# Kernel tuning notes

Hardware: AMD Instinct MI355X
Metric: run time of the kernel (lower is better)

The kernel has to match this reference:

```python
import jax, jax.numpy as jnp
import numpy as np

H, E, N, R = 1024, 2048, 16, 64  # hidden, expand, state, dt_rank
B, L = 2, 2048


def setup_inputs() -> dict:
    key = jax.random.key(0)
    ks = jax.random.split(key, 20)
    s = 0.02
    inp = {
        "x": jax.random.normal(ks[0], (B, L, H), jnp.float32),
        "ln_gamma": jnp.ones((H,), jnp.float32),
        "ln_beta": jnp.zeros((H,), jnp.float32),
        "W_in": jax.random.normal(ks[1], (H, 2 * E), jnp.float32) * s,
        "b_in": jnp.zeros((2 * E,), jnp.float32),
        "W_delta": jax.random.normal(ks[2], (E, R), jnp.float32) * s,
        "b_delta": jnp.zeros((R,), jnp.float32),
        "W_dt": jax.random.normal(ks[3], (R, E), jnp.float32) * s,
        "b_dt": jnp.zeros((E,), jnp.float32),
        "W_B": jax.random.normal(ks[4], (E, N), jnp.float32) * s,
        "b_B": jnp.zeros((N,), jnp.float32),
        "W_C": jax.random.normal(ks[5], (E, N), jnp.float32) * s,
        "b_C": jnp.zeros((N,), jnp.float32),
        "A_log": -jnp.exp(jax.random.normal(ks[6], (E, N), jnp.float32) * 0.1),
        "D": jax.random.normal(ks[7], (E,), jnp.float32) * 0.1,
        "W_out": jax.random.normal(ks[8], (E, H), jnp.float32) * s,
        "b_out": jnp.zeros((H,), jnp.float32),
    }
    return inp


def _layer_norm(x, gamma, beta, eps=1e-5):
    mu = jnp.mean(x, axis=-1, keepdims=True)
    var = jnp.var(x, axis=-1, keepdims=True)
    return (x - mu) * jax.lax.rsqrt(var + eps) * gamma + beta


def _selective_scan(x, delta, A, Bm, Cm):
    # x, delta: [B,L,E]; Bm, Cm: [B,L,N]; A: [E,N]
    def step(h, inputs):
        x_t, d_t, B_t, C_t = inputs  # [B,E],[B,E],[B,N],[B,N]
        A_disc = jnp.exp(d_t[..., None] * A)                     # [B,E,N]
        h = A_disc * h + d_t[..., None] * B_t[:, None, :] * x_t[..., None]
        y_t = jnp.einsum('bn,ben->be', C_t, h)
        return h, y_t

    h0 = jnp.zeros((x.shape[0], A.shape[0], A.shape[1]), x.dtype)
    xs = (jnp.swapaxes(x, 0, 1), jnp.swapaxes(delta, 0, 1),
          jnp.swapaxes(Bm, 0, 1), jnp.swapaxes(Cm, 0, 1))
    _, ys = jax.lax.scan(step, h0, xs)  # ys: [L,B,E]
    return jnp.swapaxes(ys, 0, 1)


def reference(x, ln_gamma, ln_beta, W_in, b_in, W_delta, b_delta, W_dt, b_dt,
              W_B, b_B, W_C, b_C, A_log, D, W_out, b_out):
    residual = x
    xn = _layer_norm(x, ln_gamma, ln_beta)
    x_proj = xn @ W_in + b_in                     # [B,L,2E]
    u, gate = jnp.split(x_proj, 2, axis=-1)
    u = jax.nn.silu(u)
    delta = jax.nn.softplus((u @ W_delta + b_delta) @ W_dt + b_dt)  # [B,L,E]
    Bm = u @ W_B + b_B                            # [B,L,N]
    Cm = u @ W_C + b_C                            # [B,L,N]
    A = -jnp.exp(A_log)                           # [E,N]
    y = _selective_scan(u, delta, A, Bm, Cm)
    y = y + u * D
    y = y * jax.nn.silu(gate)
    return y @ W_out + b_out + residual
```

## Files before the change

kernel.cpp:

```cpp
#include <hip/hip_runtime.h>
#include <stdint.h>

#define DH 1024
#define DE 2048
#define DN 16
#define DR 64
#define DB 2
#define DL 2048
#define DT (DB * DL)

typedef short short8 __attribute__((ext_vector_type(8)));
typedef float f32x4 __attribute__((ext_vector_type(4)));

__device__ __forceinline__ float bf2f(uint32_t u) {
  union { uint32_t i; float f; } v; v.i = u << 16; return v.f;
}
__device__ __forceinline__ unsigned short f2bf(float f) {
  union { float f; uint32_t i; } v; v.f = f;
  uint32_t r = v.i + 0x7FFFu + ((v.i >> 16) & 1u);
  return (unsigned short)(r >> 16);
}
__device__ __forceinline__ float ldsc(const void* p, size_t i, bool f32) {
  return f32 ? ((const float*)p)[i] : bf2f(((const unsigned short*)p)[i]);
}
__device__ __forceinline__ float4 ld4(const void* p, size_t i, bool f32) {
  if (f32) return *(const float4*)((const float*)p + i);
  ushort4 v = *(const ushort4*)((const unsigned short*)p + i);
  return make_float4(bf2f(v.x), bf2f(v.y), bf2f(v.z), bf2f(v.w));
}

__device__ __forceinline__ void gll16(const unsigned short* g, unsigned short* l) {
  __builtin_amdgcn_global_load_lds(
      (const __attribute__((address_space(1))) unsigned int*)g,
      (__attribute__((address_space(3))) unsigned int*)l, 16, 0, 0);
}

__device__ __forceinline__ void transpose_tile(
    const void* src, unsigned short* dst, int K, int N, int bx, int by,
    int tid, bool f32, float (*tile)[33]) {
  const int tx = tid & 31;
  const int ty = tid >> 5;
  const int kb = by * 32, nb = bx * 32;
  #pragma unroll
  for (int i = 0; i < 4; ++i)
    tile[ty + 8 * i][tx] = ldsc(src, (size_t)(kb + ty + 8 * i) * N + nb + tx, f32);
  __syncthreads();
  #pragma unroll
  for (int i = 0; i < 4; ++i)
    dst[(size_t)(nb + ty + 8 * i) * K + kb + tx] = f2bf(tile[tx][ty + 8 * i]);
}

__global__ __launch_bounds__(256) void k_convert_all(
    const void* __restrict__ W_in, const void* __restrict__ W_out,
    const void* __restrict__ W_dt, const void* __restrict__ Wd,
    const void* __restrict__ Wb, const void* __restrict__ Wc,
    const void* __restrict__ b_in, const void* __restrict__ b_out,
    const void* __restrict__ b_delta, const void* __restrict__ b_B,
    const void* __restrict__ b_C, const void* __restrict__ A_log,
    const void* __restrict__ Dvec, const void* __restrict__ b_dt,
    unsigned short* __restrict__ WtIn, unsigned short* __restrict__ WtOut,
    unsigned short* __restrict__ WtDt, unsigned short* __restrict__ WtDbc,
    float* __restrict__ bin, float* __restrict__ bout,
    float* __restrict__ bdbc, float* __restrict__ Ac, float* __restrict__ Dv,
    float* __restrict__ bdt,
    const uint32_t* __restrict__ probe) {
  const bool f32 = (probe[0] == 0x3F800000u);
  __shared__ float tile[32][33];
  const int tid = threadIdx.x;
  int f = blockIdx.x;
  if (f < 4096) {
    transpose_tile(W_in, WtIn, 1024, 4096, f & 127, f >> 7, tid, f32, tile);
    return;
  }
  f -= 4096;
  if (f < 2048) {
    transpose_tile(W_out, WtOut, 2048, 1024, f & 31, f >> 5, tid, f32, tile);
    return;
  }
  f -= 2048;
  if (f < 128) {
    transpose_tile(W_dt, WtDt, 64, 2048, f & 63, f >> 6, tid, f32, tile);
    return;
  }
  f -= 128;
  if (f < 1024) {
    const int idx = f * 256 + tid;
    const int c = idx >> 11, k = idx & 2047;
    float v = 0.f;
    if (c < 64) v = ldsc(Wd, (size_t)k * DR + c, f32);
    else if (c < 80) v = ldsc(Wb, (size_t)k * DN + (c - 64), f32);
    else if (c < 96) v = ldsc(Wc, (size_t)k * DN + (c - 80), f32);
    WtDbc[idx] = f2bf(v);
    return;
  }
  f -= 1024;
  {
    int i = f * 256 + tid;
    if (i < 4096) { bin[i] = ldsc(b_in, i, f32); return; }
    i -= 4096;
    if (i < 1024) { bout[i] = ldsc(b_out, i, f32); return; }
    i -= 1024;
    if (i < 128) {
      float v = 0.f;
      if (i < 64) v = ldsc(b_delta, i, f32);
      else if (i < 80) v = ldsc(b_B, i - 64, f32);
      else if (i < 96) v = ldsc(b_C, i - 80, f32);
      bdbc[i] = v; return;
    }
    i -= 128;
    if (i < 32768) { Ac[i] = -__expf(ldsc(A_log, i, f32)); return; }
    i -= 32768;
    if (i < 2048) { Dv[i] = ldsc(Dvec, i, f32); return; }
    i -= 2048;
    if (i < 2048) { bdt[i] = ldsc(b_dt, i, f32); }
  }
}

__global__ __launch_bounds__(256) void k_dbc_reduce(
    const float* __restrict__ Part, const float* __restrict__ bdbc,
    unsigned short* __restrict__ dt1b, float* __restrict__ dtBC, int MT) {
  const int gid = blockIdx.x * 256 + threadIdx.x;
  const int row = gid / 96, col = gid - row * 96;
  if (row >= MT) return;
  float s = bdbc[col];
  const size_t stride = (size_t)MT * 96;
  #pragma unroll
  for (int kp = 0; kp < 8; ++kp)
    s += Part[(size_t)kp * stride + (size_t)row * 96 + col];
  if (col < 64) dt1b[(size_t)row * 64 + col] = f2bf(s);
  else dtBC[(size_t)row * 32 + (col - 64)] = s;
}

__global__ __launch_bounds__(256) void k_delta(
    const unsigned short* __restrict__ A,
    const unsigned short* __restrict__ Wt,
    const float* __restrict__ bdt,
    unsigned short* __restrict__ Dout) {
  const int tid = threadIdx.x;
  const int wid = tid >> 6;
  const int lane = tid & 63;
  const int quad = lane >> 4;
  const int l16 = lane & 15;
  const int r0 = blockIdx.y * 32 + (wid & 1) * 16;
  const int c0 = blockIdx.x * 128 + (wid >> 1) * 64;

  const unsigned short* ap = A + (size_t)(r0 + l16) * 64 + quad * 8;
  const short8 a0 = *(const short8*)(ap);
  const short8 a1 = *(const short8*)(ap + 32);

  f32x4 acc[4];
  #pragma unroll
  for (int j = 0; j < 4; ++j) {
    acc[j][0] = 0.f; acc[j][1] = 0.f; acc[j][2] = 0.f; acc[j][3] = 0.f;
  }
  #pragma unroll
  for (int j = 0; j < 4; ++j) {
    const unsigned short* bp = Wt + (size_t)(c0 + j * 16 + l16) * 64 + quad * 8;
    const short8 b0 = *(const short8*)(bp);
    const short8 b1 = *(const short8*)(bp + 32);
    acc[j] = __builtin_amdgcn_mfma_f32_16x16x32_bf16(a0, b0, acc[j], 0, 0, 0);
    acc[j] = __builtin_amdgcn_mfma_f32_16x16x32_bf16(a1, b1, acc[j], 0, 0, 0);
  }
  #pragma unroll
  for (int j = 0; j < 4; ++j) {
    const int col = c0 + j * 16 + l16;
    const float bs = bdt[col];
    #pragma unroll
    for (int r = 0; r < 4; ++r) {
      const int row = r0 + quad * 4 + r;
      const float v = acc[j][r] + bs;
      const float sp = fmaxf(v, 0.f) + __logf(1.f + __expf(-fabsf(v)));
      Dout[(size_t)row * 2048 + col] = f2bf(sp);
    }
  }
}

__global__ __launch_bounds__(256) void k_out_reduce(
    const float* __restrict__ Part2, const float* __restrict__ bout,
    const void* __restrict__ resid, void* __restrict__ dout,
    int MT, int t0, int lgTc, const uint32_t* __restrict__ probe) {
  const bool f32 = (probe[0] == 0x3F800000u);
  const int gid = blockIdx.x * 256 + threadIdx.x;
  const int base = gid * 4;
  const int row = base >> 10;
  const int col = base & 1023;
  if (row >= MT) return;
  const int tcm = (1 << lgTc) - 1;
  const size_t grow = (size_t)((row >> lgTc) * DL + t0 + (row & tcm));
  const size_t ms = (size_t)MT * 1024;
  float4 p0 = *(const float4*)(Part2 + (size_t)row * 1024 + col);
  float4 p1 = *(const float4*)(Part2 + ms + (size_t)row * 1024 + col);
  float4 bo = *(const float4*)(bout + col);
  float4 rs = ld4(resid, grow * 1024 + col, f32);
  float4 o;
  o.x = p0.x + p1.x + bo.x + rs.x;
  o.y = p0.y + p1.y + bo.y + rs.y;
  o.z = p0.z + p1.z + bo.z + rs.z;
  o.w = p0.w + p1.w + bo.w + rs.w;
  if (f32) {
    *(float4*)((float*)dout + grow * 1024 + col) = o;
  } else {
    ushort4 u;
    u.x = f2bf(o.x); u.y = f2bf(o.y); u.z = f2bf(o.z); u.w = f2bf(o.w);
    *(ushort4*)((unsigned short*)dout + grow * 1024 + col) = u;
  }
}

__global__ __launch_bounds__(256) void ln_bf16(
    const void* __restrict__ x, const void* __restrict__ gamma,
    const void* __restrict__ beta, unsigned short* __restrict__ xn,
    int t0, int lgTc, const uint32_t* __restrict__ probe) {
  const bool f32 = (probe[0] == 0x3F800000u);
  const int row = blockIdx.x;
  const int tid = threadIdx.x;
  const int tcm = (1 << lgTc) - 1;
  const int grow = (row >> lgTc) * DL + t0 + (row & tcm);
  float4 v = ld4(x, (size_t)grow * DH + tid * 4, f32);
  float s = v.x + v.y + v.z + v.w;
  float ss = v.x * v.x + v.y * v.y + v.z * v.z + v.w * v.w;
  #pragma unroll
  for (int off = 32; off > 0; off >>= 1) {
    s += __shfl_down(s, off, 64);
    ss += __shfl_down(ss, off, 64);
  }
  __shared__ float sbuf[4], ssbuf[4];
  const int wave = tid >> 6, lane = tid & 63;
  if (lane == 0) { sbuf[wave] = s; ssbuf[wave] = ss; }
  __syncthreads();
  float tot = sbuf[0] + sbuf[1] + sbuf[2] + sbuf[3];
  float tots = ssbuf[0] + ssbuf[1] + ssbuf[2] + ssbuf[3];
  const float inv = 1.0f / (float)DH;
  float mu = tot * inv;
  float var = tots * inv - mu * mu;
  float rs = rsqrtf(var + 1e-5f);
  float4 gv = ld4(gamma, tid * 4, f32);
  float4 bv = ld4(beta, tid * 4, f32);
  ushort4 o;
  o.x = f2bf((v.x - mu) * rs * gv.x + bv.x);
  o.y = f2bf((v.y - mu) * rs * gv.y + bv.y);
  o.z = f2bf((v.z - mu) * rs * gv.z + bv.z);
  o.w = f2bf((v.w - mu) * rs * gv.w + bv.w);
  *(ushort4*)(xn + (size_t)row * DH + tid * 4) = o;
}

__global__ __launch_bounds__(256) void gemm_mfma(
    const unsigned short* __restrict__ A, int lda,
    const unsigned short* __restrict__ Wt,
    const float* __restrict__ bias,
    const void* __restrict__ resid,
    void* __restrict__ C, int ldc,
    int K, int mode, int t0, int lgTc,
    const uint32_t* __restrict__ probe) {
  __shared__ unsigned short As[2][4096];
  __shared__ unsigned short Bs[2][4096];
  const int tid = threadIdx.x;
  const int wid = tid >> 6;
  const int lane = tid & 63;
  const int quad = lane >> 4;
  const int l16 = lane & 15;
  const int wm = (wid & 1) * 64;
  const int wn = (wid >> 1) * 64;
  const int m0 = blockIdx.y * 128;
  int n0 = blockIdx.x * 128;
  int kbeg = 0, kend = K;
  if (mode == 5) {
    const int Ks = K >> 3; kbeg = blockIdx.x * Ks; kend = kbeg + Ks; n0 = 0;
  } else if (mode == 6) {
    const int Ks = K >> 1; const int kp = blockIdx.x >> 3;
    kbeg = kp * Ks; kend = kbeg + Ks; n0 = (blockIdx.x & 7) * 128;
  }
  const int sr = tid >> 2;
  const int sc = (tid & 3) * 8;

  const unsigned short* gA0 = A + (size_t)(m0 + sr) * lda + sc;
  const unsigned short* gA1 = A + (size_t)(m0 + sr + 64) * lda + sc;
  const unsigned short* gB0 = Wt + (size_t)(n0 + sr) * K + sc;
  const unsigned short* gB1 = Wt + (size_t)(n0 + sr + 64) * K + sc;
  const int wb = (tid & 192) * 8;
  unsigned short* lA00 = &As[0][wb];
  unsigned short* lA01 = &As[1][wb];
  unsigned short* lA10 = &As[0][2048 + wb];
  unsigned short* lA11 = &As[1][2048 + wb];
  unsigned short* lB00 = &Bs[0][wb];
  unsigned short* lB01 = &Bs[1][wb];
  unsigned short* lB10 = &Bs[0][2048 + wb];
  unsigned short* lB11 = &Bs[1][2048 + wb];

  f32x4 acc[4][4];
  #pragma unroll
  for (int i = 0; i < 4; ++i)
    #pragma unroll
    for (int j = 0; j < 4; ++j) {
      acc[i][j][0] = 0.f; acc[i][j][1] = 0.f;
      acc[i][j][2] = 0.f; acc[i][j][3] = 0.f;
    }

  for (int k0 = kbeg; k0 < kend; k0 += 64) {
    gll16(gA0 + k0, lA00);
    gll16(gA0 + k0 + 32, lA01);
    gll16(gA1 + k0, lA10);
    gll16(gA1 + k0 + 32, lA11);
    gll16(gB0 + k0, lB00);
    gll16(gB0 + k0 + 32, lB01);
    gll16(gB1 + k0, lB10);
    gll16(gB1 + k0 + 32, lB11);
    __syncthreads();
    #pragma unroll
    for (int ks = 0; ks < 2; ++ks) {
      short8 af[4], bf[4];
      #pragma unroll
      for (int i = 0; i < 4; ++i)
        af[i] = *(const short8*)(&As[ks][(wm + i * 16 + l16) * 32 + quad * 8]);
      #pragma unroll
      for (int j = 0; j < 4; ++j)
        bf[j] = *(const short8*)(&Bs[ks][(wn + j * 16 + l16) * 32 + quad * 8]);
      #pragma unroll
      for (int i = 0; i < 4; ++i)
        #pragma unroll
        for (int j = 0; j < 4; ++j)
          acc[i][j] = __builtin_amdgcn_mfma_f32_16x16x32_bf16(af[i], bf[j], acc[i][j], 0, 0, 0);
    }
    __syncthreads();
  }

  const int tcm = (1 << lgTc) - 1;
  const bool f32 = (probe[0] == 0x3F800000u);
  #pragma unroll
  for (int i = 0; i < 4; ++i) {
    #pragma unroll
    for (int j = 0; j < 4; ++j) {
      const int col = n0 + wn + j * 16 + l16;
      const float bsv = (mode == 5 || mode == 6) ? 0.f : bias[col];
      #pragma unroll
      for (int r = 0; r < 4; ++r) {
        const int row = m0 + wm + i * 16 + quad * 4 + r;
        float v = acc[i][j][r] + bsv;
        if (mode == 1) {
          if (col < DE) v = v / (1.f + __expf(-v));
          ((unsigned short*)C)[(size_t)row * ldc + col] = f2bf(v);
        } else if (mode == 2) {
          v = (v > 15.0f) ? v : log1pf(__expf(v));
          ((unsigned short*)C)[(size_t)row * ldc + col] = f2bf(v);
        } else if (mode == 5) {
          if (col < 96) {
            const size_t kpb = (size_t)blockIdx.x * ((size_t)gridDim.y * 128) * 96;
            ((float*)C)[kpb + (size_t)row * 96 + col] = v;
          }
        } else if (mode == 6) {
          const size_t kpb = (size_t)(blockIdx.x >> 3) * ((size_t)gridDim.y * 128) * 1024;
          ((float*)C)[kpb + (size_t)row * 1024 + col] = v;
        } else {
          const size_t grow = (size_t)((row >> lgTc) * DL + t0 + (row & tcm));
          v += ldsc(resid, grow * ldc + col, f32);
          if (f32) ((float*)C)[grow * ldc + col] = v;
          else ((unsigned short*)C)[grow * ldc + col] = f2bf(v);
        }
      }
    }
  }
}

__global__ __launch_bounds__(256) void scan_phaseA(
    const unsigned short* __restrict__ xproj,
    const unsigned short* __restrict__ delta,
    const float* __restrict__ dtBC,
    const float* __restrict__ Ac,
    float* __restrict__ Aprod,
    float* __restrict__ Hpart,
    int Tc, int P) {
  const int tid = threadIdx.x;
  const int ng = tid & 3;
  const int e = blockIdx.x * 64 + (tid >> 2);
  const int bs = blockIdx.y;
  const int S = Tc / P;
  const int b = bs / S, s = bs - b * S;
  const int r0 = b * Tc + s * P;

  const float4 ac = *(const float4*)(Ac + (size_t)e * 16 + ng * 4);
  const unsigned short* dp = delta + (size_t)r0 * 2048 + e;
  const unsigned short* xp = xproj + (size_t)r0 * 4096 + e;
  const float* bp = dtBC + (size_t)r0 * 32 + ng * 4;

  float4 ap = make_float4(1.f, 1.f, 1.f, 1.f);
  float4 h = make_float4(0.f, 0.f, 0.f, 0.f);
  for (int t = 0; t < P; ++t) {
    const float d = bf2f(*dp);
    const float x = bf2f(*xp);
    const float4 B = *(const float4*)bp;
    const float a0 = __expf(d * ac.x), a1 = __expf(d * ac.y),
                a2 = __expf(d * ac.z), a3 = __expf(d * ac.w);
    ap.x *= a0; ap.y *= a1; ap.z *= a2; ap.w *= a3;
    const float dx = d * x;
    h.x = a0 * h.x + dx * B.x;
    h.y = a1 * h.y + dx * B.y;
    h.z = a2 * h.z + dx * B.z;
    h.w = a3 * h.w + dx * B.w;
    dp += 2048; xp += 4096; bp += 32;
  }
  const size_t o = ((size_t)bs * 2048 + e) * 16 + ng * 4;
  *(float4*)(Aprod + o) = ap;
  *(float4*)(Hpart + o) = h;
}

__global__ __launch_bounds__(256) void scan_phaseB(
    const float* __restrict__ Aprod, const float* __restrict__ Hpart,
    float* __restrict__ Hstart,
    float* __restrict__ hstate,
    int S, int first) {
  const int gid = blockIdx.x * 256 + threadIdx.x;
  const int b = gid >> 13;
  const int en4 = gid & 8191;
  float4 h = first ? make_float4(0.f, 0.f, 0.f, 0.f)
                   : ((const float4*)hstate)[gid];
  for (int s = 0; s < S; ++s) {
    const size_t o = ((size_t)(b * S + s) << 13) + en4;
    ((float4*)Hstart)[o] = h;
    const float4 a = ((const float4*)Aprod)[o];
    const float4 p = ((const float4*)Hpart)[o];
    h.x = a.x * h.x + p.x;
    h.y = a.y * h.y + p.y;
    h.z = a.z * h.z + p.z;
    h.w = a.w * h.w + p.w;
  }
  ((float4*)hstate)[gid] = h;
}

__global__ __launch_bounds__(256) void scan_phaseC(
    unsigned short* __restrict__ xproj,
    const unsigned short* __restrict__ delta,
    const float* __restrict__ dtBC,
    const float* __restrict__ Ac,
    const float* __restrict__ Dv,
    const float* __restrict__ Hstart,
    int Tc, int P) {
  const int tid = threadIdx.x;
  const int ng = tid & 3;
  const int e = blockIdx.x * 64 + (tid >> 2);
  const int bs = blockIdx.y;
  const int S = Tc / P;
  const int b = bs / S, s = bs - b * S;
  const int r0 = b * Tc + s * P;

  const float4 ac = *(const float4*)(Ac + (size_t)e * 16 + ng * 4);
  const float dv = Dv[e];
  float4 h = *(const float4*)(Hstart + ((size_t)bs * 2048 + e) * 16 + ng * 4);

  const unsigned short* dp = delta + (size_t)r0 * 2048 + e;
  unsigned short* xp = xproj + (size_t)r0 * 4096 + e;
  const float* bp = dtBC + (size_t)r0 * 32 + ng * 4;

  for (int t = 0; t < P; ++t) {
    const float d = bf2f(*dp);
    const float x = bf2f(xp[0]);
    const float4 B = *(const float4*)bp;
    const float4 Cc = *(const float4*)(bp + 16);
    const float a0 = __expf(d * ac.x), a1 = __expf(d * ac.y),
                a2 = __expf(d * ac.z), a3 = __expf(d * ac.w);
    const float dx = d * x;
    h.x = a0 * h.x + dx * B.x;
    h.y = a1 * h.y + dx * B.y;
    h.z = a2 * h.z + dx * B.z;
    h.w = a3 * h.w + dx * B.w;
    float y = h.x * Cc.x + h.y * Cc.y + h.z * Cc.z + h.w * Cc.w;
    y += __shfl_xor(y, 1, 64);
    y += __shfl_xor(y, 2, 64);
    const float g = bf2f(xp[2048]);
    const float sg = g / (1.f + __expf(-g));
    const unsigned short outv = f2bf((y + x * dv) * sg);
    if (ng == 0) xp[2048] = outv;
    dp += 2048; xp += 4096; bp += 32;
  }
}

__global__ __launch_bounds__(256) void ln_kernel(
    const void* __restrict__ x, const void* __restrict__ gamma,
    const void* __restrict__ beta, float* __restrict__ xn,
    int t0, int lgTc, const uint32_t* __restrict__ probe) {
  const bool f32 = (probe[0] == 0x3F800000u);
  const int row = blockIdx.x;
  const int tid = threadIdx.x;
  const int tcm = (1 << lgTc) - 1;
  const int grow = (row >> lgTc) * DL + t0 + (row & tcm);
  float4 v = ld4(x, (size_t)grow * DH + tid * 4, f32);
  float s = v.x + v.y + v.z + v.w;
  float ss = v.x * v.x + v.y * v.y + v.z * v.z + v.w * v.w;
  #pragma unroll
  for (int off = 32; off > 0; off >>= 1) {
    s += __shfl_down(s, off, 64);
    ss += __shfl_down(ss, off, 64);
  }
  __shared__ float sbuf[4], ssbuf[4];
  const int wave = tid >> 6, lane = tid & 63;
  if (lane == 0) { sbuf[wave] = s; ssbuf[wave] = ss; }
  __syncthreads();
  float tot = sbuf[0] + sbuf[1] + sbuf[2] + sbuf[3];
  float tots = ssbuf[0] + ssbuf[1] + ssbuf[2] + ssbuf[3];
  const float inv = 1.0f / (float)DH;
  float mu = tot * inv;
  float var = tots * inv - mu * mu;
  float rs = rsqrtf(var + 1e-5f);
  float4 gv = ld4(gamma, tid * 4, f32);
  float4 bv = ld4(beta, tid * 4, f32);
  float4 o;
  o.x = (v.x - mu) * rs * gv.x + bv.x;
  o.y = (v.y - mu) * rs * gv.y + bv.y;
  o.z = (v.z - mu) * rs * gv.z + bv.z;
  o.w = (v.w - mu) * rs * gv.w + bv.w;
  *(float4*)(xn + (size_t)row * DH + tid * 4) = o;
}

#define BM 64
#define BN 64
#define BK 16
__global__ __launch_bounds__(256) void gemm_k(
    const float* __restrict__ A, int lda,
    const void* __restrict__ W,
    const void* __restrict__ bias,
    const void* __restrict__ resid,
    void* __restrict__ C, int ldc, int c_output,
    int N, int K, int mode, int t0, int lgTc,
    const uint32_t* __restrict__ probe) {
  const bool f32 = (probe[0] == 0x3F800000u);
  __shared__ float As[BM][BK + 1];
  __shared__ float Bs[BK][BN + 4];
  const int tid = threadIdx.x;
  const int tx = tid & 15;
  const int ty = tid >> 4;
  const int m0 = blockIdx.y * BM;
  const int n0 = blockIdx.x * BN;
  const int aRow = tid >> 2;
  const int aCol = (tid & 3) << 2;
  const int bRow = tid >> 4;
  const int bCol = (tid & 15) << 2;

  float acc[4][4];
  #pragma unroll
  for (int i = 0; i < 4; ++i)
    #pragma unroll
    for (int j = 0; j < 4; ++j) acc[i][j] = 0.f;

  for (int k0 = 0; k0 < K; k0 += BK) {
    float4 av = *(const float4*)(A + (size_t)(m0 + aRow) * lda + (k0 + aCol));
    As[aRow][aCol + 0] = av.x;
    As[aRow][aCol + 1] = av.y;
    As[aRow][aCol + 2] = av.z;
    As[aRow][aCol + 3] = av.w;
    if (n0 + bCol < N) {
      float4 bv = ld4(W, (size_t)(k0 + bRow) * N + (n0 + bCol), f32);
      Bs[bRow][bCol + 0] = bv.x;
      Bs[bRow][bCol + 1] = bv.y;
      Bs[bRow][bCol + 2] = bv.z;
      Bs[bRow][bCol + 3] = bv.w;
    } else {
      Bs[bRow][bCol + 0] = 0.f;
      Bs[bRow][bCol + 1] = 0.f;
      Bs[bRow][bCol + 2] = 0.f;
      Bs[bRow][bCol + 3] = 0.f;
    }
    __syncthreads();
    #pragma unroll
    for (int k = 0; k < BK; ++k) {
      float a0 = As[ty * 4 + 0][k];
      float a1 = As[ty * 4 + 1][k];
      float a2 = As[ty * 4 + 2][k];
      float a3 = As[ty * 4 + 3][k];
      float b0 = Bs[k][tx * 4 + 0];
      float b1 = Bs[k][tx * 4 + 1];
      float b2 = Bs[k][tx * 4 + 2];
      float b3 = Bs[k][tx * 4 + 3];
      acc[0][0] += a0 * b0; acc[0][1] += a0 * b1; acc[0][2] += a0 * b2; acc[0][3] += a0 * b3;
      acc[1][0] += a1 * b0; acc[1][1] += a1 * b1; acc[1][2] += a1 * b2; acc[1][3] += a1 * b3;
      acc[2][0] += a2 * b0; acc[2][1] += a2 * b1; acc[2][2] += a2 * b2; acc[2][3] += a2 * b3;
      acc[3][0] += a3 * b0; acc[3][1] += a3 * b1; acc[3][2] += a3 * b2; acc[3][3] += a3 * b3;
    }
    __syncthreads();
  }

  const int tcm = (1 << lgTc) - 1;
  #pragma unroll
  for (int i = 0; i < 4; ++i) {
    const int gm = m0 + ty * 4 + i;
    #pragma unroll
    for (int j = 0; j < 4; ++j) {
      const int gn = n0 + tx * 4 + j;
      if (gn < N) {
        float v = acc[i][j] + ldsc(bias, gn, f32);
        size_t crow = (size_t)gm;
        if (mode == 1) {
          if (gn < DE) v = v / (1.0f + __expf(-v));
        } else if (mode == 2) {
          v = (v > 15.0f) ? v : log1pf(__expf(v));
        } else if (mode == 3) {
          const size_t grow = (size_t)((gm >> lgTc) * DL + t0 + (gm & tcm));
          v += ldsc(resid, grow * ldc + gn, f32);
          crow = grow;
        }
        if (c_output) {
          if (f32) ((float*)C)[crow * ldc + gn] = v;
          else ((unsigned short*)C)[crow * ldc + gn] = f2bf(v);
        } else {
          ((float*)C)[crow * ldc + gn] = v;
        }
      }
    }
  }
}

__global__ __launch_bounds__(256) void scan_kernel(
    float* __restrict__ xproj, const float* __restrict__ delta,
    const float* __restrict__ Bmat, const float* __restrict__ Cmat,
    const void* __restrict__ A_log, const void* __restrict__ Dvec,
    float* __restrict__ hstate, int Tc, int first,
    const uint32_t* __restrict__ probe) {
  const bool f32 = (probe[0] == 0x3F800000u);
  const int gid = blockIdx.x * 256 + threadIdx.x;
  const int b = gid >> 11;
  const int e = gid & (DE - 1);
  float Ac[DN];
  #pragma unroll
  for (int n = 0; n < DN; ++n) Ac[n] = -__expf(ldsc(A_log, (size_t)e * DN + n, f32));
  const float Dvl = ldsc(Dvec, e, f32);
  float h[DN];
  float* hs = hstate + ((size_t)b * DE + e) * DN;
  if (first) {
    #pragma unroll
    for (int n = 0; n < DN; ++n) h[n] = 0.f;
  } else {
    #pragma unroll
    for (int n = 0; n < DN; ++n) h[n] = hs[n];
  }
  for (int t = 0; t < Tc; ++t) {
    const size_t r = (size_t)(b * Tc + t);
    const float x = xproj[r * (2 * DE) + e];
    const float g = xproj[r * (2 * DE) + DE + e];
    const float d = delta[r * DE + e];
    const float4* bp = (const float4*)(Bmat + r * DN);
    const float4* cp = (const float4*)(Cmat + r * DN);
    float4 b0 = bp[0], b1 = bp[1], b2 = bp[2], b3 = bp[3];
    float4 c0 = cp[0], c1 = cp[1], c2 = cp[2], c3 = cp[3];
    float Bv[DN] = {b0.x,b0.y,b0.z,b0.w, b1.x,b1.y,b1.z,b1.w,
                    b2.x,b2.y,b2.z,b2.w, b3.x,b3.y,b3.z,b3.w};
    float Cv[DN] = {c0.x,c0.y,c0.z,c0.w, c1.x,c1.y,c1.z,c1.w,
                    c2.x,c2.y,c2.z,c2.w, c3.x,c3.y,c3.z,c3.w};
    const float dx = d * x;
    float y = 0.f;
    #pragma unroll
    for (int n = 0; n < DN; ++n) {
      float ad = __expf(d * Ac[n]);
      h[n] = ad * h[n] + dx * Bv[n];
      y += Cv[n] * h[n];
    }
    const float sg = g / (1.0f + __expf(-g));
    xproj[r * (2 * DE) + DE + e] = (y + x * Dvl) * sg;
  }
  #pragma unroll
  for (int n = 0; n < DN; ++n) hs[n] = h[n];
}

extern "C" void kernel_launch(void* const* d_in, const int* in_sizes, int n_in,
                              void* d_out, int out_size, void* d_ws, size_t ws_size,
                              hipStream_t stream) {
  const void* x = d_in[0];
  const void* ln_gamma = d_in[1];
  const void* ln_beta = d_in[2];
  const void* W_in = d_in[3];
  const void* b_in = d_in[4];
  const void* W_delta = d_in[5];
  const void* b_delta = d_in[6];
  const void* W_dt = d_in[7];
  const void* b_dt = d_in[8];
  const void* W_B = d_in[9];
  const void* b_B = d_in[10];
  const void* W_C = d_in[11];
  const void* b_C = d_in[12];
  const void* A_log = d_in[13];
  const void* Dvec = d_in[14];
  const void* W_out = d_in[15];
  const void* b_out = d_in[16];
  const uint32_t* probe = (const uint32_t*)ln_gamma;
  char* ws = (char*)d_ws;

  const size_t P_WTIN = (size_t)4096 * 1024 * 2;
  const size_t P_WTOUT = (size_t)1024 * 2048 * 2;
  const size_t P_WDBC = (size_t)128 * 2048 * 2;
  const size_t P_WDT = (size_t)2048 * 64 * 2;
  const size_t P_F32 = (size_t)(4096 + 1024 + 128 + 32768 + 2048 + 2048 + 65536) * 4;
  const size_t persist = P_WTIN + P_WTOUT + P_WDBC + P_WDT + P_F32;
  auto chunk_bytes = [](int Tc) {
    const int P = Tc < 64 ? Tc : 64;
    const size_t S = (size_t)(Tc / P);
    const size_t MT = (size_t)DB * Tc;
    size_t tail = MT * (2048 * 2 + 8 * 96 * 4) + 3 * (size_t)DB * S * 32768 * 4;
    size_t part2 = MT * 8192;
    if (part2 > tail) tail = part2;
    return MT * ((1024 + 4096 + 64) * 2 + 32 * 4) + tail;
  };
  int lgTc = -1;
  for (int lg = 11; lg >= 6; --lg) {
    if (persist + chunk_bytes(1 << lg) + 4096 <= ws_size) { lgTc = lg; break; }
  }

  if (lgTc >= 0) {
    const int Tc = 1 << lgTc;
    const int MT = DB * Tc;
    const int nchunks = DL / Tc;
    const int P = Tc < 64 ? Tc : 64;
    const int S = Tc / P;

    size_t off = 0;
    unsigned short* WtIn = (unsigned short*)(ws + off); off += P_WTIN;
    unsigned short* WtOut = (unsigned short*)(ws + off); off += P_WTOUT;
    unsigned short* WtDbc = (unsigned short*)(ws + off); off += P_WDBC;
    unsigned short* WtDt = (unsigned short*)(ws + off); off += P_WDT;
    float* bin = (float*)(ws + off); off += 4096 * 4;
    float* bout = (float*)(ws + off); off += 1024 * 4;
    float* bdbc = (float*)(ws + off); off += 128 * 4;
    float* bdt = (float*)(ws + off); off += 2048 * 4;
    float* Ac = (float*)(ws + off); off += 32768 * 4;
    float* Dv = (float*)(ws + off); off += 2048 * 4;
    float* hstate = (float*)(ws + off); off += 65536 * 4;
    unsigned short* xn = (unsigned short*)(ws + off); off += (size_t)MT * 1024 * 2;
    unsigned short* xproj = (unsigned short*)(ws + off); off += (size_t)MT * 4096 * 2;
    unsigned short* dt1b = (unsigned short*)(ws + off); off += (size_t)MT * 64 * 2;
    float* dtBC = (float*)(ws + off); off += (size_t)MT * 32 * 4;
    char* alias0 = ws + off;
    unsigned short* delta = (unsigned short*)(alias0);
    float* Part = (float*)(alias0 + (size_t)MT * 2048 * 2);
    float* Aprod = (float*)(alias0 + (size_t)MT * 2048 * 2 + (size_t)8 * MT * 96 * 4);
    float* Hpart = Aprod + (size_t)DB * S * 32768;
    float* Hstart = Hpart + (size_t)DB * S * 32768;
    float* Part2 = (float*)(alias0);

    k_convert_all<<<7469, 256, 0, stream>>>(
        W_in, W_out, W_dt, W_delta, W_B, W_C,
        b_in, b_out, b_delta, b_B, b_C, A_log, Dvec, b_dt,
        WtIn, WtOut, WtDt, WtDbc, bin, bout, bdbc, Ac, Dv, bdt, probe);

    for (int c = 0; c < nchunks; ++c) {
      const int t0 = c * Tc;
      ln_bf16<<<MT, 256, 0, stream>>>(x, ln_gamma, ln_beta, xn, t0, lgTc, probe);
      gemm_mfma<<<dim3(4096 / 128, MT / 128), 256, 0, stream>>>(
          xn, 1024, WtIn, bin, nullptr, xproj, 4096, 1024, 1, 0, 0, probe);
      gemm_mfma<<<dim3(8, MT / 128), 256, 0, stream>>>(
          xproj, 4096, WtDbc, bdbc, nullptr, Part, 96, 2048, 5, 0, 0, probe);
      k_dbc_reduce<<<(MT * 96 + 255) / 256, 256, 0, stream>>>(
          Part, bdbc, dt1b, dtBC, MT);
      k_delta<<<dim3(2048 / 128, MT / 32), 256, 0, stream>>>(
          dt1b, WtDt, bdt, delta);
      scan_phaseA<<<dim3(32, DB * S), 256, 0, stream>>>(
          xproj, delta, dtBC, Ac, Aprod, Hpart, Tc, P);
      scan_phaseB<<<64, 256, 0, stream>>>(
          Aprod, Hpart, Hstart, hstate, S, c == 0 ? 1 : 0);
      scan_phaseC<<<dim3(32, DB * S), 256, 0, stream>>>(
          xproj, delta, dtBC, Ac, Dv, Hstart, Tc, P);
      gemm_mfma<<<dim3(16, MT / 128), 256, 0, stream>>>(
          xproj + DE, 4096, WtOut, bout, nullptr, Part2, 1024, 2048, 6, 0, 0, probe);
      k_out_reduce<<<MT, 256, 0, stream>>>(
          Part2, bout, x, d_out, MT, t0, lgTc, probe);
    }
    return;
  }

  {
    int lg = 8;
    while (lg > 6 &&
           ((size_t)(2u << lg) * 7264 * 4 + (size_t)DB * DE * DN * 4 + 4096) > ws_size)
      --lg;
    const int Tc = 1 << lg;
    const int MT = DB * Tc;
    const int nchunks = DL / Tc;

    size_t off = 0;
    float* xproj_c = (float*)(ws + off); off += (size_t)MT * 2 * DE * 4;
    float* xn_c    = (float*)(ws + off); off += (size_t)MT * DH * 4;
    float* delta_c = (float*)(ws + off); off += (size_t)MT * DE * 4;
    float* dt1_c   = (float*)(ws + off); off += (size_t)MT * DR * 4;
    float* Bm_c    = (float*)(ws + off); off += (size_t)MT * DN * 4;
    float* Cm_c    = (float*)(ws + off); off += (size_t)MT * DN * 4;
    float* hstate  = (float*)(ws + off);

    for (int c = 0; c < nchunks; ++c) {
      const int t0 = c * Tc;
      ln_kernel<<<MT, 256, 0, stream>>>(x, ln_gamma, ln_beta, xn_c, t0, lg, probe);
      gemm_k<<<dim3(2 * DE / BN, MT / BM), 256, 0, stream>>>(
          xn_c, DH, W_in, b_in, nullptr, xproj_c, 2 * DE, 0, 2 * DE, DH, 1, 0, 0, probe);
      gemm_k<<<dim3(1, MT / BM), 256, 0, stream>>>(
          xproj_c, 2 * DE, W_delta, b_delta, nullptr, dt1_c, DR, 0, DR, DE, 0, 0, 0, probe);
      gemm_k<<<dim3(DE / BN, MT / BM), 256, 0, stream>>>(
          dt1_c, DR, W_dt, b_dt, nullptr, delta_c, DE, 0, DE, DR, 2, 0, 0, probe);
      gemm_k<<<dim3(1, MT / BM), 256, 0, stream>>>(
          xproj_c, 2 * DE, W_B, b_B, nullptr, Bm_c, DN, 0, DN, DE, 0, 0, 0, probe);
      gemm_k<<<dim3(1, MT / BM), 256, 0, stream>>>(
          xproj_c, 2 * DE, W_C, b_C, nullptr, Cm_c, DN, 0, DN, DE, 0, 0, 0, probe);
      scan_kernel<<<16, 256, 0, stream>>>(
          xproj_c, delta_c, Bm_c, Cm_c, A_log, Dvec, hstate, Tc, c == 0 ? 1 : 0, probe);
      gemm_k<<<dim3(DH / BN, MT / BM), 256, 0, stream>>>(
          xproj_c + DE, 2 * DE, W_out, b_out, x, d_out, DH, 1, DH, DE, 3, t0, lg, probe);
    }
  }
}
```

Measured before the change: 432.3 us.

## Remap GEMM LDS tiles to fragment-major layout and swizzle workgroup order across XCDs

The GEMM now stages A and B tiles in LDS so that each 16x32 MFMA fragment is contiguous. A lane's short8 read becomes a linear lane*8 access, which is meant to remove LDS bank conflicts on fragment loads. The workgroup ID is also remapped so that consecutive blocks on the same XCD cover neighbouring tiles, aiming for better L2 reuse on the multi-XCD MI355X. The global loads become 16-row by 8-column strided per wave, which may coalesce less well than the previous row-contiguous pattern.

```diff
diff --git a/kernel.cpp b/kernel.cpp
--- a/kernel.cpp
+++ b/kernel.cpp
@@ -251,8 +251,8 @@
     void* __restrict__ C, int ldc,
     int K, int mode, int t0, int lgTc,
     const uint32_t* __restrict__ probe) {
-  __shared__ unsigned short As[2][4096];
-  __shared__ unsigned short Bs[2][4096];
+  __shared__ unsigned short As[8192];
+  __shared__ unsigned short Bs[8192];
   const int tid = threadIdx.x;
   const int wid = tid >> 6;
   const int lane = tid & 63;
@@ -260,31 +260,36 @@
   const int l16 = lane & 15;
   const int wm = (wid & 1) * 64;
   const int wn = (wid >> 1) * 64;
-  const int m0 = blockIdx.y * 128;
-  int n0 = blockIdx.x * 128;
+
+  const int nbx = gridDim.x;
+  const int nwg = nbx * (int)gridDim.y;
+  int id = blockIdx.y * nbx + blockIdx.x;
+  if ((nwg & 7) == 0) id = (id & 7) * (nwg >> 3) + (id >> 3);
+  const int bxs = id % nbx;
+  const int m0 = (id / nbx) * 128;
+  int n0 = bxs * 128;
   int kbeg = 0, kend = K;
   if (mode == 5) {
-    const int Ks = K >> 3; kbeg = blockIdx.x * Ks; kend = kbeg + Ks; n0 = 0;
+    const int Ks = K >> 3; kbeg = bxs * Ks; kend = kbeg + Ks; n0 = 0;
   } else if (mode == 6) {
-    const int Ks = K >> 1; const int kp = blockIdx.x >> 3;
-    kbeg = kp * Ks; kend = kbeg + Ks; n0 = (blockIdx.x & 7) * 128;
-  }
-  const int sr = tid >> 2;
-  const int sc = (tid & 3) * 8;
-
-  const unsigned short* gA0 = A + (size_t)(m0 + sr) * lda + sc;
-  const unsigned short* gA1 = A + (size_t)(m0 + sr + 64) * lda + sc;
-  const unsigned short* gB0 = Wt + (size_t)(n0 + sr) * K + sc;
-  const unsigned short* gB1 = Wt + (size_t)(n0 + sr + 64) * K + sc;
-  const int wb = (tid & 192) * 8;
-  unsigned short* lA00 = &As[0][wb];
-  unsigned short* lA01 = &As[1][wb];
-  unsigned short* lA10 = &As[0][2048 + wb];
-  unsigned short* lA11 = &As[1][2048 + wb];
-  unsigned short* lB00 = &Bs[0][wb];
-  unsigned short* lB01 = &Bs[1][wb];
-  unsigned short* lB10 = &Bs[0][2048 + wb];
-  unsigned short* lB11 = &Bs[1][2048 + wb];
+    const int Ks = K >> 1; const int kp = bxs >> 3;
+    kbeg = kp * Ks; kend = kbeg + Ks; n0 = (bxs & 7) * 128;
+  }
+
+  const unsigned short* gAsrc[4];
+  const unsigned short* gBsrc[4];
+  unsigned short* lAdst[4];
+  unsigned short* lBdst[4];
+  #pragma unroll
+  for (int q = 0; q < 4; ++q) {
+    const int fb = wid * 4 + q;
+    const int fr = (fb >> 1) * 16 + l16;
+    const int fc = (fb & 1) * 32 + quad * 8;
+    gAsrc[q] = A + (size_t)(m0 + fr) * lda + fc;
+    gBsrc[q] = Wt + (size_t)(n0 + fr) * K + fc;
+    lAdst[q] = &As[fb * 512];
+    lBdst[q] = &Bs[fb * 512];
+  }
 
   f32x4 acc[4][4];
   #pragma unroll
@@ -296,24 +301,21 @@
     }
 
   for (int k0 = kbeg; k0 < kend; k0 += 64) {
-    gll16(gA0 + k0, lA00);
-    gll16(gA0 + k0 + 32, lA01);
-    gll16(gA1 + k0, lA10);
-    gll16(gA1 + k0 + 32, lA11);
-    gll16(gB0 + k0, lB00);
-    gll16(gB0 + k0 + 32, lB01);
-    gll16(gB1 + k0, lB10);
-    gll16(gB1 + k0 + 32, lB11);
+    #pragma unroll
+    for (int q = 0; q < 4; ++q) {
+      gll16(gAsrc[q] + k0, lAdst[q]);
+      gll16(gBsrc[q] + k0, lBdst[q]);
+    }
     __syncthreads();
     #pragma unroll
     for (int ks = 0; ks < 2; ++ks) {
       short8 af[4], bf[4];
       #pragma unroll
       for (int i = 0; i < 4; ++i)
-        af[i] = *(const short8*)(&As[ks][(wm + i * 16 + l16) * 32 + quad * 8]);
+        af[i] = *(const short8*)(&As[((((wm >> 4) + i) * 2 + ks) << 9) + lane * 8]);
       #pragma unroll
       for (int j = 0; j < 4; ++j)
-        bf[j] = *(const short8*)(&Bs[ks][(wn + j * 16 + l16) * 32 + quad * 8]);
+        bf[j] = *(const short8*)(&Bs[((((wn >> 4) + j) * 2 + ks) << 9) + lane * 8]);
       #pragma unroll
       for (int i = 0; i < 4; ++i)
         #pragma unroll
@@ -343,11 +345,11 @@
           ((unsigned short*)C)[(size_t)row * ldc + col] = f2bf(v);
         } else if (mode == 5) {
           if (col < 96) {
-            const size_t kpb = (size_t)blockIdx.x * ((size_t)gridDim.y * 128) * 96;
+            const size_t kpb = (size_t)bxs * ((size_t)gridDim.y * 128) * 96;
             ((float*)C)[kpb + (size_t)row * 96 + col] = v;
           }
         } else if (mode == 6) {
-          const size_t kpb = (size_t)(blockIdx.x >> 3) * ((size_t)gridDim.y * 128) * 1024;
+          const size_t kpb = (size_t)(bxs >> 3) * ((size_t)gridDim.y * 128) * 1024;
           ((float*)C)[kpb + (size_t)row * 1024 + col] = v;
         } else {
           const size_t grow = (size_t)((row >> lgTc) * DL + t0 + (row & tcm));
```

After: 471.0 us. +8.9%, slower.

## Assign one channel per thread with all 16 states in scan phases A and C

Applied to the files above, without the earlier changes.

The selective-scan phase A and C kernels now give each thread one expand channel holding all 16 state values in registers, instead of spreading each channel over 4 threads with 4 states each. This removes the cross-lane shuffle reduction for y and the redundant per-lane loads of delta, x and gate. Every lane in a wave now touches a distinct channel, so bf16 loads and stores are coalesced. The cost is four times fewer threads and blocks per chunk (grid x drops from 32 to 8) and higher register pressure, which may hurt occupancy and latency hiding.

```diff
diff --git a/kernel.cpp b/kernel.cpp
--- a/kernel.cpp
+++ b/kernel.cpp
@@ -368,38 +368,51 @@
     float* __restrict__ Aprod,
     float* __restrict__ Hpart,
     int Tc, int P) {
-  const int tid = threadIdx.x;
-  const int ng = tid & 3;
-  const int e = blockIdx.x * 64 + (tid >> 2);
+  const int e = blockIdx.x * 256 + threadIdx.x;
   const int bs = blockIdx.y;
   const int S = Tc / P;
   const int b = bs / S, s = bs - b * S;
   const int r0 = b * Tc + s * P;
 
-  const float4 ac = *(const float4*)(Ac + (size_t)e * 16 + ng * 4);
+  float ac[16], ap[16], h[16];
+  #pragma unroll
+  for (int g = 0; g < 4; ++g) {
+    const float4 a4 = *(const float4*)(Ac + (size_t)e * 16 + g * 4);
+    ac[g * 4 + 0] = a4.x; ac[g * 4 + 1] = a4.y;
+    ac[g * 4 + 2] = a4.z; ac[g * 4 + 3] = a4.w;
+  }
+  #pragma unroll
+  for (int n = 0; n < 16; ++n) { ap[n] = 1.f; h[n] = 0.f; }
+
   const unsigned short* dp = delta + (size_t)r0 * 2048 + e;
   const unsigned short* xp = xproj + (size_t)r0 * 4096 + e;
-  const float* bp = dtBC + (size_t)r0 * 32 + ng * 4;
-
-  float4 ap = make_float4(1.f, 1.f, 1.f, 1.f);
-  float4 h = make_float4(0.f, 0.f, 0.f, 0.f);
+  const float* bp = dtBC + (size_t)r0 * 32;
+
   for (int t = 0; t < P; ++t) {
     const float d = bf2f(*dp);
     const float x = bf2f(*xp);
-    const float4 B = *(const float4*)bp;
-    const float a0 = __expf(d * ac.x), a1 = __expf(d * ac.y),
-                a2 = __expf(d * ac.z), a3 = __expf(d * ac.w);
-    ap.x *= a0; ap.y *= a1; ap.z *= a2; ap.w *= a3;
     const float dx = d * x;
-    h.x = a0 * h.x + dx * B.x;
-    h.y = a1 * h.y + dx * B.y;
-    h.z = a2 * h.z + dx * B.z;
-    h.w = a3 * h.w + dx * B.w;
+    #pragma unroll
+    for (int g = 0; g < 4; ++g) {
+      const float4 B = *(const float4*)(bp + g * 4);
+      const float Bv[4] = {B.x, B.y, B.z, B.w};
+      #pragma unroll
+      for (int q = 0; q < 4; ++q) {
+        const int n = g * 4 + q;
+        const float a = __expf(d * ac[n]);
+        ap[n] *= a;
+        h[n] = a * h[n] + dx * Bv[q];
+      }
+    }
     dp += 2048; xp += 4096; bp += 32;
   }
-  const size_t o = ((size_t)bs * 2048 + e) * 16 + ng * 4;
-  *(float4*)(Aprod + o) = ap;
-  *(float4*)(Hpart + o) = h;
+  float* oA = Aprod + ((size_t)bs * 2048 + e) * 16;
+  float* oH = Hpart + ((size_t)bs * 2048 + e) * 16;
+  #pragma unroll
+  for (int g = 0; g < 4; ++g) {
+    *(float4*)(oA + g * 4) = make_float4(ap[g*4+0], ap[g*4+1], ap[g*4+2], ap[g*4+3]);
+    *(float4*)(oH + g * 4) = make_float4(h[g*4+0], h[g*4+1], h[g*4+2], h[g*4+3]);
+  }
 }
 
 __global__ __launch_bounds__(256) void scan_phaseB(
@@ -433,41 +446,50 @@
     const float* __restrict__ Dv,
     const float* __restrict__ Hstart,
     int Tc, int P) {
-  const int tid = threadIdx.x;
-  const int ng = tid & 3;
-  const int e = blockIdx.x * 64 + (tid >> 2);
+  const int e = blockIdx.x * 256 + threadIdx.x;
   const int bs = blockIdx.y;
   const int S = Tc / P;
   const int b = bs / S, s = bs - b * S;
   const int r0 = b * Tc + s * P;
 
-  const float4 ac = *(const float4*)(Ac + (size_t)e * 16 + ng * 4);
+  float ac[16], h[16];
+  #pragma unroll
+  for (int g = 0; g < 4; ++g) {
+    const float4 a4 = *(const float4*)(Ac + (size_t)e * 16 + g * 4);
+    ac[g * 4 + 0] = a4.x; ac[g * 4 + 1] = a4.y;
+    ac[g * 4 + 2] = a4.z; ac[g * 4 + 3] = a4.w;
+    const float4 h4 = *(const float4*)(Hstart + ((size_t)bs * 2048 + e) * 16 + g * 4);
+    h[g * 4 + 0] = h4.x; h[g * 4 + 1] = h4.y;
+    h[g * 4 + 2] = h4.z; h[g * 4 + 3] = h4.w;
+  }
   const float dv = Dv[e];
-  float4 h = *(const float4*)(Hstart + ((size_t)bs * 2048 + e) * 16 + ng * 4);
 
   const unsigned short* dp = delta + (size_t)r0 * 2048 + e;
   unsigned short* xp = xproj + (size_t)r0 * 4096 + e;
-  const float* bp = dtBC + (size_t)r0 * 32 + ng * 4;
+  const float* bp = dtBC + (size_t)r0 * 32;
 
   for (int t = 0; t < P; ++t) {
     const float d = bf2f(*dp);
     const float x = bf2f(xp[0]);
-    const float4 B = *(const float4*)bp;
-    const float4 Cc = *(const float4*)(bp + 16);
-    const float a0 = __expf(d * ac.x), a1 = __expf(d * ac.y),
-                a2 = __expf(d * ac.z), a3 = __expf(d * ac.w);
     const float dx = d * x;
-    h.x = a0 * h.x + dx * B.x;
-    h.y = a1 * h.y + dx * B.y;
-    h.z = a2 * h.z + dx * B.z;
-    h.w = a3 * h.w + dx * B.w;
-    float y = h.x * Cc.x + h.y * Cc.y + h.z * Cc.z + h.w * Cc.w;
-    y += __shfl_xor(y, 1, 64);
-    y += __shfl_xor(y, 2, 64);
+    float y = 0.f;
+    #pragma unroll
+    for (int g = 0; g < 4; ++g) {
+      const float4 B = *(const float4*)(bp + g * 4);
+      const float4 Cc = *(const float4*)(bp + 16 + g * 4);
+      const float Bv[4] = {B.x, B.y, B.z, B.w};
+      const float Cv[4] = {Cc.x, Cc.y, Cc.z, Cc.w};
+      #pragma unroll
+      for (int q = 0; q < 4; ++q) {
+        const int n = g * 4 + q;
+        const float a = __expf(d * ac[n]);
+        h[n] = a * h[n] + dx * Bv[q];
+        y += Cv[q] * h[n];
+      }
+    }
     const float g = bf2f(xp[2048]);
     const float sg = g / (1.f + __expf(-g));
-    const unsigned short outv = f2bf((y + x * dv) * sg);
-    if (ng == 0) xp[2048] = outv;
+    xp[2048] = f2bf((y + x * dv) * sg);
     dp += 2048; xp += 4096; bp += 32;
   }
 }
@@ -747,11 +769,11 @@
           Part, bdbc, dt1b, dtBC, MT);
       k_delta<<<dim3(2048 / 128, MT / 32), 256, 0, stream>>>(
           dt1b, WtDt, bdt, delta);
-      scan_phaseA<<<dim3(32, DB * S), 256, 0, stream>>>(
+      scan_phaseA<<<dim3(2048 / 256, DB * S), 256, 0, stream>>>(
           xproj, delta, dtBC, Ac, Aprod, Hpart, Tc, P);
       scan_phaseB<<<64, 256, 0, stream>>>(
           Aprod, Hpart, Hstart, hstate, S, c == 0 ? 1 : 0);
-      scan_phaseC<<<dim3(32, DB * S), 256, 0, stream>>>(
+      scan_phaseC<<<dim3(2048 / 256, DB * S), 256, 0, stream>>>(
           xproj, delta, dtBC, Ac, Dv, Hstart, Tc, P);
       gemm_mfma<<<dim3(16, MT / 128), 256, 0, stream>>>(
           xproj + DE, 4096, WtOut, bout, nullptr, Part2, 1024, 2048, 6, 0, 0, probe);
```

Measured after the change: 409.0 us. -5.4%, faster.
